# Optimization experiments

Hardware: AMD Instinct MI355X
Metric: run time of the kernel (lower is better)

Reference implementation:

```python
import jax, jax.numpy as jnp
import numpy as np

# SigKernel config (from init_kwargs)
SCALES = np.array([1.0], dtype=np.float32)
S0, S1 = 0.0, 1.0   # s0, S
T0, T1 = 0.0, 1.0   # t0, T
REFINEMENT = 1.0    # refinement_factor (new grid == old grid => interp is identity)


def _interpolate(X, t_min, t_max, refinement_factor):
    """Linear interpolation of batched paths (B, L, D) onto a refined uniform grid."""
    L = X.shape[1]
    new_L = int(refinement_factor * (L - 1)) + 1
    t = jnp.linspace(t_min, t_max, L)
    t_new = jnp.linspace(t_min, t_max, new_L)
    interp_ch = lambda ch: jnp.interp(t_new, t, ch)            # (L,) -> (new_L,)
    interp_path = lambda p: jax.vmap(interp_ch, in_axes=1, out_axes=1)(p)
    return jax.vmap(interp_path)(X)


def _solve_pde_single(inc):
    """Second-order finite-difference Goursat solve of K_st = inc * K.

    inc: (m, m) increment matrix. Returns K[m, m] (scalar), with boundary K[i,0]=K[0,j]=1.
    Wavefront recursion over the 2m-1 interior antidiagonals via lax.scan; each
    diagonal is stored as a length-(m+1) vector indexed by the row i (col j = d - i).
    """
    m = inc.shape[0]
    n = m + 1
    idx = jnp.arange(n)
    K0 = jnp.where(idx == 0, 1.0, 0.0)   # antidiagonal d=0
    K1 = jnp.where(idx <= 1, 1.0, 0.0)   # antidiagonal d=1

    def step(carry, d):
        Km2, Km1 = carry                 # diagonals d-2, d-1
        j = d - idx
        ir = jnp.clip(idx - 1, 0, m - 1)
        jc = jnp.clip(j - 1, 0, m - 1)
        a = inc[ir, jc]                  # inc[i-1, j-1] along the diagonal
        f1 = 1.0 + 0.5 * a + (a * a) * (1.0 / 12.0)
        f2 = 1.0 - (a * a) * (1.0 / 12.0)
        # K[i,j] = (K[i,j-1] + K[i-1,j]) * f1 - K[i-1,j-1] * f2
        Kij = (Km1 + jnp.roll(Km1, 1)) * f1 - jnp.roll(Km2, 1) * f2
        Kd = jnp.where((idx == 0) | (j == 0), 1.0, Kij)      # boundary = 1
        Kd = jnp.where((j >= 0) & (j <= m), Kd, 0.0)         # off-diagonal mask
        return (Km1, Kd), None

    (_, Klast), _ = jax.lax.scan(step, (K0, K1), jnp.arange(2, 2 * m + 1))
    return Klast[m]  # K at (m, m)


def _sig_kernel_matrix(X, Y, scale):
    # linear static kernel k(x,y) = scale^2 <x,y>  =>  grid increments of k
    dX = X[:, 1:, :] - X[:, :-1, :]   # (bx, m, d)
    dY = Y[:, 1:, :] - Y[:, :-1, :]   # (by, m, d)
    inc = (scale * scale) * jnp.einsum('aic,bjc->abij', dX, dY)  # (bx, by, m, m)
    return jax.vmap(jax.vmap(_solve_pde_single))(inc)            # (bx, by)


def reference(X, Y):
    Xi = _interpolate(X, S0, S1, REFINEMENT)
    Yi = _interpolate(Y, T0, T1, REFINEMENT)
    scales = jnp.asarray(SCALES)
    ks = jax.vmap(lambda s: _sig_kernel_matrix(Xi, Yi, s))(scales)
    return jnp.mean(ks, axis=0)


def setup_inputs() -> dict:
    key = jax.random.key(0)
    kx, ky = jax.random.split(key)
    bx, by, L, d = 32, 32, 256, 8
    # 0.05 scaling keeps the (exponentially growing) PDE solution well-conditioned
    X = 0.05 * jax.random.normal(kx, (bx, L, d), dtype=jnp.float32)
    Y = 0.05 * jax.random.normal(ky, (by, L, d), dtype=jnp.float32)
    return {"X": X, "Y": Y}
```

## Files before the change

kernel.cpp:

```cpp
#include <hip/hip_runtime.h>


typedef float f32x2 __attribute__((ext_vector_type(2)));
typedef float f32x4 __attribute__((ext_vector_type(4)));

#define MM   255
#define DYST 9
#define DYSZ 3456

static __device__ inline f32x2 fma2(f32x2 a, f32x2 b, f32x2 c) {
    return __builtin_elementwise_fma(a, b, c);
}

static __device__ inline float shr1_or_one(float x) {
    int r = __builtin_amdgcn_update_dpp(
        __float_as_int(1.0f), __float_as_int(x),
        0x138 , 0xF, 0xF, false);
    return __int_as_float(r);
}

__global__ __launch_bounds__(64) void sigker_dpp(
    const float* __restrict__ X,
    const float* __restrict__ Y,
    float* __restrict__ out)
{
    const int pair = blockIdx.x;
    const int ax = pair >> 5;
    const int by = pair & 31;
    const int l  = threadIdx.x;

    __shared__ float dYs[DYSZ];

    const float* Xa = X + ax * 2048;
    const float* Yb = Y + by * 2048;

    {
        f32x4* dz = (f32x4*)dYs;
        #pragma unroll
        for (int v = l; v < DYSZ / 4; v += 64) dz[v] = (f32x4){0, 0, 0, 0};
    }
    __syncthreads();
    for (int v = l; v < MM * 8; v += 64) {
        const int j = v >> 3, c = v & 7;
        dYs[(j + 63) * DYST + c] = Yb[(j + 1) * 8 + c] - Yb[j * 8 + c];
    }

    f32x2 dxp0[8], dxp1[8];
    {
        f32x4 f[10];
        const f32x4* Xv = (const f32x4*)(Xa + l * 32);
        #pragma unroll
        for (int k = 0; k < 8; ++k) f[k] = Xv[k];
        f[8] = (l < 63) ? Xv[8] : (f32x4){0, 0, 0, 0};
        f[9] = (l < 63) ? Xv[9] : (f32x4){0, 0, 0, 0};
        #pragma unroll
        for (int c = 0; c < 8; ++c) {
            const float e0 = f[(c)      >> 2][(c)      & 3];
            const float e1 = f[(8 + c)  >> 2][(8 + c)  & 3];
            const float e2 = f[(16 + c) >> 2][(16 + c) & 3];
            const float e3 = f[(24 + c) >> 2][(24 + c) & 3];
            const float e4 = f[(32 + c) >> 2][(32 + c) & 3];
            dxp0[c] = (f32x2){e1 - e0, e2 - e1};
            dxp1[c] = (f32x2){e3 - e2, e4 - e3};
        }
    }
    __syncthreads();

    const f32x2 C12  = { 1.0f / 12.0f,  1.0f / 12.0f};
    const f32x2 CN12 = {-1.0f / 12.0f, -1.0f / 12.0f};
    const f32x2 CH   = { 0.5f, 0.5f};
    const f32x2 C1   = { 1.0f, 1.0f};

    auto factors = [&](const float* dy, f32x2& f1a, f32x2& f1b,
                       f32x2& f2a, f32x2& f2b) {
        f32x2 b = (f32x2){dy[0], dy[0]};
        f32x2 a01 = dxp0[0] * b, a23 = dxp1[0] * b;
        #pragma unroll
        for (int c = 1; c < 8; ++c) {
            b = (f32x2){dy[c], dy[c]};
            a01 = fma2(dxp0[c], b, a01);
            a23 = fma2(dxp1[c], b, a23);
        }
        const f32x2 q01 = a01 * a01, q23 = a23 * a23;
        f1a = fma2(q01, C12, fma2(a01, CH, C1));
        f1b = fma2(q23, C12, fma2(a23, CH, C1));
        f2a = fma2(q01, CN12, C1);
        f2b = fma2(q23, CN12, C1);
    };

    float K0 = 1.0f, K1 = 1.0f, K2 = 1.0f, K3 = 1.0f, upd = 1.0f;

    const int base = (63 - l) * DYST;
    float dyN[8];
    f32x2 f1a, f1b, f2a, f2b;
    {
        float dyA[8];
        #pragma unroll
        for (int c = 0; c < 8; ++c) dyA[c] = dYs[base + c];
        factors(dyA, f1a, f1b, f2a, f2b);
        #pragma unroll
        for (int c = 0; c < 8; ++c) dyN[c] = dYs[base + DYST + c];
    }
    int pbase = base + 2 * DYST;

    #pragma unroll 2
    for (int s = 1; s <= MM + 63; ++s) {
        float dyP[8];
        #pragma unroll
        for (int c = 0; c < 8; ++c) dyP[c] = dYs[pbase + c];

        const float up = shr1_or_one(K3);

        const float t0 = upd * f2a.x;
        const float t1 = K0  * f2a.y;
        const float t2 = K1  * f2b.x;
        const float t3 = K2  * f2b.y;
        const float c0 = fmaf(K0, f1a.x, -t0);
        const float c1 = fmaf(K1, f1a.y, -t1);
        const float c2 = fmaf(K2, f1b.x, -t2);
        const float c3 = fmaf(K3, f1b.y, -t3);

        const float k0 = fmaf(up, f1a.x, c0);
        const float k1 = fmaf(k0, f1a.y, c1);
        const float k2 = fmaf(k1, f1b.x, c2);
        const float k3 = fmaf(k2, f1b.y, c3);

        upd = up; K0 = k0; K1 = k1; K2 = k2; K3 = k3;

        factors(dyN, f1a, f1b, f2a, f2b);

        #pragma unroll
        for (int c = 0; c < 8; ++c) dyN[c] = dyP[c];
        pbase += DYST;
    }

    if (l == 63) out[pair] = K2;
}

extern "C" void kernel_launch(void* const* d_in, const int* in_sizes, int n_in,
                              void* d_out, int out_size, void* d_ws, size_t ws_size,
                              hipStream_t stream)
{
    const float* X = (const float*)d_in[0];
    const float* Y = (const float*)d_in[1];
    float* out = (float*)d_out;
    (void)in_sizes; (void)n_in; (void)out_size; (void)d_ws; (void)ws_size;

    sigker_dpp<<<dim3(32 * 32), dim3(64), 0, stream>>>(X, Y, out);
}
```

Baseline: 41.03 us.

## Stream dY rows across lanes with DPP shifts instead of per-lane LDS reads

Each lane no longer reads its own dY row from shared memory every wavefront step. Lane 0 now loads the next row with broadcast float4 reads, and the other lanes take their row from the neighbouring lane through DPP row-shift moves. The dY staging also changes: it is computed from vectorised global loads into a compact float4 layout, replacing the padded strided layout with its zero-fill pass. This cuts per-lane LDS traffic and address arithmetic, but adds eight DPP moves and eight selects per step to the serial, VALU-bound recurrence loop.

```diff
diff --git a/kernel.cpp b/kernel.cpp
--- a/kernel.cpp
+++ b/kernel.cpp
@@ -4,9 +4,9 @@
 typedef float f32x2 __attribute__((ext_vector_type(2)));
 typedef float f32x4 __attribute__((ext_vector_type(4)));
 
-#define MM   255
-#define DYST 9
-#define DYSZ 3456
+#define MM    255
+#define NINC  255
+#define DYCOLS 324
 
 static __device__ inline f32x2 fma2(f32x2 a, f32x2 b, f32x2 c) {
     return __builtin_elementwise_fma(a, b, c);
@@ -19,7 +19,14 @@
     return __int_as_float(r);
 }
 
-__global__ __launch_bounds__(64) void sigker_dpp(
+static __device__ inline float shr1_keep(float x) {
+    int r = __builtin_amdgcn_update_dpp(
+        __float_as_int(x), __float_as_int(x),
+        0x138 , 0xF, 0xF, false);
+    return __int_as_float(r);
+}
+
+__global__ __launch_bounds__(64) void sigker_dppstream(
     const float* __restrict__ X,
     const float* __restrict__ Y,
     float* __restrict__ out)
@@ -29,20 +36,40 @@
     const int by = pair & 31;
     const int l  = threadIdx.x;
 
-    __shared__ float dYs[DYSZ];
+    __shared__ f32x4 dYv[DYCOLS * 2];
 
     const float* Xa = X + ax * 2048;
     const float* Yb = Y + by * 2048;
 
+    for (int v = l; v < (DYCOLS - NINC) * 2; v += 64)
+        dYv[NINC * 2 + v] = (f32x4){0, 0, 0, 0};
+
     {
-        f32x4* dz = (f32x4*)dYs;
+        f32x4 g[10];
+        const f32x4* Yv = (const f32x4*)(Yb + l * 32);
         #pragma unroll
-        for (int v = l; v < DYSZ / 4; v += 64) dz[v] = (f32x4){0, 0, 0, 0};
-    }
-    __syncthreads();
-    for (int v = l; v < MM * 8; v += 64) {
-        const int j = v >> 3, c = v & 7;
-        dYs[(j + 63) * DYST + c] = Yb[(j + 1) * 8 + c] - Yb[j * 8 + c];
+        for (int k = 0; k < 8; ++k) g[k] = Yv[k];
+        g[8] = (l < 63) ? Yv[8] : (f32x4){0, 0, 0, 0};
+        g[9] = (l < 63) ? Yv[9] : (f32x4){0, 0, 0, 0};
+        #pragma unroll
+        for (int r = 0; r < 4; ++r) {
+            const int ji = 4 * l + r;
+            if (ji < NINC) {
+                f32x4 d0, d1;
+                #pragma unroll
+                for (int c = 0; c < 4; ++c) {
+                    const int e = r * 8 + c;
+                    d0[c] = g[(e + 8) >> 2][(e + 8) & 3] - g[e >> 2][e & 3];
+                }
+                #pragma unroll
+                for (int c = 4; c < 8; ++c) {
+                    const int e = r * 8 + c;
+                    d1[c - 4] = g[(e + 8) >> 2][(e + 8) & 3] - g[e >> 2][e & 3];
+                }
+                dYv[2 * ji]     = d0;
+                dYv[2 * ji + 1] = d1;
+            }
+        }
     }
 
     f32x2 dxp0[8], dxp1[8];
@@ -71,16 +98,19 @@
     const f32x2 CH   = { 0.5f, 0.5f};
     const f32x2 C1   = { 1.0f, 1.0f};
 
-    auto factors = [&](const float* dy, f32x2& f1a, f32x2& f1b,
-                       f32x2& f2a, f32x2& f2b) {
-        f32x2 b = (f32x2){dy[0], dy[0]};
+    float dy0, dy1, dy2, dy3, dy4, dy5, dy6, dy7;
+    f32x2 f1a, f1b, f2a, f2b;
+
+    auto factors = [&]() {
+        f32x2 b = (f32x2){dy0, dy0};
         f32x2 a01 = dxp0[0] * b, a23 = dxp1[0] * b;
-        #pragma unroll
-        for (int c = 1; c < 8; ++c) {
-            b = (f32x2){dy[c], dy[c]};
-            a01 = fma2(dxp0[c], b, a01);
-            a23 = fma2(dxp1[c], b, a23);
-        }
+        b = (f32x2){dy1, dy1}; a01 = fma2(dxp0[1], b, a01); a23 = fma2(dxp1[1], b, a23);
+        b = (f32x2){dy2, dy2}; a01 = fma2(dxp0[2], b, a01); a23 = fma2(dxp1[2], b, a23);
+        b = (f32x2){dy3, dy3}; a01 = fma2(dxp0[3], b, a01); a23 = fma2(dxp1[3], b, a23);
+        b = (f32x2){dy4, dy4}; a01 = fma2(dxp0[4], b, a01); a23 = fma2(dxp1[4], b, a23);
+        b = (f32x2){dy5, dy5}; a01 = fma2(dxp0[5], b, a01); a23 = fma2(dxp1[5], b, a23);
+        b = (f32x2){dy6, dy6}; a01 = fma2(dxp0[6], b, a01); a23 = fma2(dxp1[6], b, a23);
+        b = (f32x2){dy7, dy7}; a01 = fma2(dxp0[7], b, a01); a23 = fma2(dxp1[7], b, a23);
         const f32x2 q01 = a01 * a01, q23 = a23 * a23;
         f1a = fma2(q01, C12, fma2(a01, CH, C1));
         f1b = fma2(q23, C12, fma2(a23, CH, C1));
@@ -88,29 +118,27 @@
         f2b = fma2(q23, CN12, C1);
     };
 
+    const bool isL0 = (l == 0);
+
+    {
+        const f32x4 i0 = dYv[0], i1 = dYv[1];
+        dy0 = isL0 ? i0.x : 0.0f; dy1 = isL0 ? i0.y : 0.0f;
+        dy2 = isL0 ? i0.z : 0.0f; dy3 = isL0 ? i0.w : 0.0f;
+        dy4 = isL0 ? i1.x : 0.0f; dy5 = isL0 ? i1.y : 0.0f;
+        dy6 = isL0 ? i1.z : 0.0f; dy7 = isL0 ? i1.w : 0.0f;
+    }
+    factors();
+
+    f32x4 bcA = dYv[2], bcB = dYv[3];
+
     float K0 = 1.0f, K1 = 1.0f, K2 = 1.0f, K3 = 1.0f, upd = 1.0f;
-
-    const int base = (63 - l) * DYST;
-    float dyN[8];
-    f32x2 f1a, f1b, f2a, f2b;
-    {
-        float dyA[8];
-        #pragma unroll
-        for (int c = 0; c < 8; ++c) dyA[c] = dYs[base + c];
-        factors(dyA, f1a, f1b, f2a, f2b);
-        #pragma unroll
-        for (int c = 0; c < 8; ++c) dyN[c] = dYs[base + DYST + c];
-    }
-    int pbase = base + 2 * DYST;
 
     #pragma unroll 2
     for (int s = 1; s <= MM + 63; ++s) {
-        float dyP[8];
-        #pragma unroll
-        for (int c = 0; c < 8; ++c) dyP[c] = dYs[pbase + c];
+        const f32x4 nA = dYv[2 * s + 2];
+        const f32x4 nB = dYv[2 * s + 3];
 
         const float up = shr1_or_one(K3);
-
         const float t0 = upd * f2a.x;
         const float t1 = K0  * f2a.y;
         const float t2 = K1  * f2b.x;
@@ -119,19 +147,24 @@
         const float c1 = fmaf(K1, f1a.y, -t1);
         const float c2 = fmaf(K2, f1b.x, -t2);
         const float c3 = fmaf(K3, f1b.y, -t3);
-
         const float k0 = fmaf(up, f1a.x, c0);
         const float k1 = fmaf(k0, f1a.y, c1);
         const float k2 = fmaf(k1, f1b.x, c2);
         const float k3 = fmaf(k2, f1b.y, c3);
-
         upd = up; K0 = k0; K1 = k1; K2 = k2; K3 = k3;
 
-        factors(dyN, f1a, f1b, f2a, f2b);
+        dy0 = shr1_keep(dy0); dy1 = shr1_keep(dy1);
+        dy2 = shr1_keep(dy2); dy3 = shr1_keep(dy3);
+        dy4 = shr1_keep(dy4); dy5 = shr1_keep(dy5);
+        dy6 = shr1_keep(dy6); dy7 = shr1_keep(dy7);
+        dy0 = isL0 ? bcA.x : dy0; dy1 = isL0 ? bcA.y : dy1;
+        dy2 = isL0 ? bcA.z : dy2; dy3 = isL0 ? bcA.w : dy3;
+        dy4 = isL0 ? bcB.x : dy4; dy5 = isL0 ? bcB.y : dy5;
+        dy6 = isL0 ? bcB.z : dy6; dy7 = isL0 ? bcB.w : dy7;
 
-        #pragma unroll
-        for (int c = 0; c < 8; ++c) dyN[c] = dyP[c];
-        pbase += DYST;
+        factors();
+
+        bcA = nA; bcB = nB;
     }
 
     if (l == 63) out[pair] = K2;
@@ -146,5 +179,5 @@
     float* out = (float*)d_out;
     (void)in_sizes; (void)n_in; (void)out_size; (void)d_ws; (void)ws_size;
 
-    sigker_dpp<<<dim3(32 * 32), dim3(64), 0, stream>>>(X, Y, out);
+    sigker_dppstream<<<dim3(32 * 32), dim3(64), 0, stream>>>(X, Y, out);
 }
```

Result: slower. 44.01 us (+7.3%).

## Pipeline factor computation two steps ahead with packed-broadcast inline asm

Applied to the files above, without the earlier changes.

Restructures the wavefront loop into a 3-way rotated register pipeline: the dY row is loaded three steps ahead and the f1/f2 factors are built two steps ahead, so the serial K recurrence no longer waits on the factor computation. The dot-product uses inline v_pk_fma_f32 with op_sel broadcast, which avoids separate scalar-to-pair broadcast moves, and splits the accumulation into two chains that are summed at the end. Costs more registers, and the loop is hand-unrolled by 3 with a fixed trip count of 106*3=318, which matches MM+63.

```diff
diff --git a/kernel.cpp b/kernel.cpp
--- a/kernel.cpp
+++ b/kernel.cpp
@@ -12,14 +12,28 @@
     return __builtin_elementwise_fma(a, b, c);
 }
 
-static __device__ inline float shr1_or_one(float x) {
+static __device__ inline float dpp_shr1(float old, float x) {
     int r = __builtin_amdgcn_update_dpp(
-        __float_as_int(1.0f), __float_as_int(x),
-        0x138 , 0xF, 0xF, false);
+        __float_as_int(old), __float_as_int(x), 0x138, 0xF, 0xF, false);
     return __int_as_float(r);
 }
 
-__global__ __launch_bounds__(64) void sigker_dpp(
+static __device__ inline void pk_mul_bl(f32x2& d, f32x2 a, f32x2 b) {
+    asm("v_pk_mul_f32 %0, %1, %2 op_sel:[0,0] op_sel_hi:[1,0]"
+        : "=v"(d) : "v"(a), "v"(b));
+}
+static __device__ inline void pk_fma_bl(f32x2& d, f32x2 a, f32x2 b) {
+    asm("v_pk_fma_f32 %0, %1, %2, %0 op_sel:[0,0,0] op_sel_hi:[1,0,1]"
+        : "+v"(d) : "v"(a), "v"(b));
+}
+static __device__ inline void pk_fma_bh(f32x2& d, f32x2 a, f32x2 b) {
+    asm("v_pk_fma_f32 %0, %1, %2, %0 op_sel:[0,1,0] op_sel_hi:[1,1,1]"
+        : "+v"(d) : "v"(a), "v"(b));
+}
+
+struct Fset { f32x2 f1a, f1b, f2a, f2b; };
+
+__global__ __launch_bounds__(64) void sigker_pipe2(
     const float* __restrict__ X,
     const float* __restrict__ Y,
     float* __restrict__ out)
@@ -71,70 +85,76 @@
     const f32x2 CH   = { 0.5f, 0.5f};
     const f32x2 C1   = { 1.0f, 1.0f};
 
-    auto factors = [&](const float* dy, f32x2& f1a, f32x2& f1b,
-                       f32x2& f2a, f32x2& f2b) {
-        f32x2 b = (f32x2){dy[0], dy[0]};
-        f32x2 a01 = dxp0[0] * b, a23 = dxp1[0] * b;
-        #pragma unroll
-        for (int c = 1; c < 8; ++c) {
-            b = (f32x2){dy[c], dy[c]};
-            a01 = fma2(dxp0[c], b, a01);
-            a23 = fma2(dxp1[c], b, a23);
-        }
-        const f32x2 q01 = a01 * a01, q23 = a23 * a23;
-        f1a = fma2(q01, C12, fma2(a01, CH, C1));
-        f1b = fma2(q23, C12, fma2(a23, CH, C1));
-        f2a = fma2(q01, CN12, C1);
-        f2b = fma2(q23, CN12, C1);
-    };
+    const int base = (63 - l) * DYST;
 
+#define LOADDY(D, P) do {                                                    \
+    D[0].x = (P)[0]; D[0].y = (P)[1];                                        \
+    D[1].x = (P)[2]; D[1].y = (P)[3];                                        \
+    D[2].x = (P)[4]; D[2].y = (P)[5];                                        \
+    D[3].x = (P)[6]; D[3].y = (P)[7];                                        \
+} while (0)
+
+#define BUILD(FB, D) do {                                                    \
+    f32x2 A0_, A1_, B0_, B1_;                                                \
+    pk_mul_bl(A0_, dxp0[0], D[0]);  pk_mul_bl(B0_, dxp1[0], D[0]);           \
+    pk_fma_bh(A0_, dxp0[1], D[0]);  pk_fma_bh(B0_, dxp1[1], D[0]);           \
+    pk_fma_bl(A0_, dxp0[2], D[1]);  pk_fma_bl(B0_, dxp1[2], D[1]);           \
+    pk_fma_bh(A0_, dxp0[3], D[1]);  pk_fma_bh(B0_, dxp1[3], D[1]);           \
+    pk_mul_bl(A1_, dxp0[4], D[2]);  pk_mul_bl(B1_, dxp1[4], D[2]);           \
+    pk_fma_bh(A1_, dxp0[5], D[2]);  pk_fma_bh(B1_, dxp1[5], D[2]);           \
+    pk_fma_bl(A1_, dxp0[6], D[3]);  pk_fma_bl(B1_, dxp1[6], D[3]);           \
+    pk_fma_bh(A1_, dxp0[7], D[3]);  pk_fma_bh(B1_, dxp1[7], D[3]);           \
+    const f32x2 a01_ = A0_ + A1_;                                            \
+    const f32x2 a23_ = B0_ + B1_;                                            \
+    const f32x2 q01_ = a01_ * a01_, q23_ = a23_ * a23_;                      \
+    FB.f1a = fma2(q01_, C12, fma2(a01_, CH, C1));                            \
+    FB.f1b = fma2(q23_, C12, fma2(a23_, CH, C1));                            \
+    FB.f2a = fma2(q01_, CN12, C1);                                           \
+    FB.f2b = fma2(q23_, CN12, C1);                                           \
+} while (0)
+
+#define STEP(DLD, DCS, FU, FB) do {                                          \
+    LOADDY(DLD, pld); pld += DYST;                                           \
+    const float up_ = dpp_shr1(1.0f, K3);                                    \
+    const float t0_ = upd * FU.f2a.x;                                        \
+    const float t1_ = K0  * FU.f2a.y;                                        \
+    const float t2_ = K1  * FU.f2b.x;                                        \
+    const float t3_ = K2  * FU.f2b.y;                                        \
+    const float c0_ = fmaf(K0, FU.f1a.x, -t0_);                              \
+    const float c1_ = fmaf(K1, FU.f1a.y, -t1_);                              \
+    const float c2_ = fmaf(K2, FU.f1b.x, -t2_);                              \
+    const float c3_ = fmaf(K3, FU.f1b.y, -t3_);                              \
+    const float k0_ = fmaf(up_, FU.f1a.x, c0_);                              \
+    const float k1_ = fmaf(k0_, FU.f1a.y, c1_);                              \
+    const float k2_ = fmaf(k1_, FU.f1b.x, c2_);                              \
+    const float k3_ = fmaf(k2_, FU.f1b.y, c3_);                              \
+    upd = up_; K0 = k0_; K1 = k1_; K2 = k2_; K3 = k3_;                       \
+    BUILD(FB, DCS);                                                          \
+} while (0)
+
+    f32x2 DA[4], DB[4], DC[4];
+    Fset F0, F1, F2;
     float K0 = 1.0f, K1 = 1.0f, K2 = 1.0f, K3 = 1.0f, upd = 1.0f;
 
-    const int base = (63 - l) * DYST;
-    float dyN[8];
-    f32x2 f1a, f1b, f2a, f2b;
-    {
-        float dyA[8];
-        #pragma unroll
-        for (int c = 0; c < 8; ++c) dyA[c] = dYs[base + c];
-        factors(dyA, f1a, f1b, f2a, f2b);
-        #pragma unroll
-        for (int c = 0; c < 8; ++c) dyN[c] = dYs[base + DYST + c];
-    }
-    int pbase = base + 2 * DYST;
+    LOADDY(DB, dYs + base);
+    LOADDY(DC, dYs + base + DYST);
+    LOADDY(DA, dYs + base + 2 * DYST);
+    BUILD(F0, DB);
+    BUILD(F1, DC);
+    const float* pld = dYs + base + 3 * DYST;
 
-    #pragma unroll 2
-    for (int s = 1; s <= MM + 63; ++s) {
-        float dyP[8];
-        #pragma unroll
-        for (int c = 0; c < 8; ++c) dyP[c] = dYs[pbase + c];
-
-        const float up = shr1_or_one(K3);
-
-        const float t0 = upd * f2a.x;
-        const float t1 = K0  * f2a.y;
-        const float t2 = K1  * f2b.x;
-        const float t3 = K2  * f2b.y;
-        const float c0 = fmaf(K0, f1a.x, -t0);
-        const float c1 = fmaf(K1, f1a.y, -t1);
-        const float c2 = fmaf(K2, f1b.x, -t2);
-        const float c3 = fmaf(K3, f1b.y, -t3);
-
-        const float k0 = fmaf(up, f1a.x, c0);
-        const float k1 = fmaf(k0, f1a.y, c1);
-        const float k2 = fmaf(k1, f1b.x, c2);
-        const float k3 = fmaf(k2, f1b.y, c3);
-
-        upd = up; K0 = k0; K1 = k1; K2 = k2; K3 = k3;
-
-        factors(dyN, f1a, f1b, f2a, f2b);
-
-        #pragma unroll
-        for (int c = 0; c < 8; ++c) dyN[c] = dyP[c];
-        pbase += DYST;
+    #pragma unroll 1
+    for (int it = 0; it < 106; ++it) {
+        STEP(DB, DA, F0, F2);
+        STEP(DC, DB, F1, F0);
+        STEP(DA, DC, F2, F1);
     }
 
     if (l == 63) out[pair] = K2;
+
+#undef STEP
+#undef BUILD
+#undef LOADDY
 }
 
 extern "C" void kernel_launch(void* const* d_in, const int* in_sizes, int n_in,
@@ -146,5 +166,5 @@
     float* out = (float*)d_out;
     (void)in_sizes; (void)n_in; (void)out_size; (void)d_ws; (void)ws_size;
 
-    sigker_dpp<<<dim3(32 * 32), dim3(64), 0, stream>>>(X, Y, out);
+    sigker_pipe2<<<dim3(32 * 32), dim3(64), 0, stream>>>(X, Y, out);
 }
```

After: 39.17 us. 4.5% less time.
